# Performance work log

Measured on AMD Instinct MI355X. Metric: run time of the kernel, lower is better.

The kernel has to match this reference:

```python
import jax, jax.numpy as jnp
import numpy as np

B = 16384          # batch
F = 64             # number of feature columns (tables)
L = 10             # pooled lookups per feature (bag size)
E = 16             # embedding dim
V = 1_000_000      # hashed vocab size (shared table)
D = F * E          # concat width = 1024
EPS = 1e-5


def setup_inputs() -> dict:
    key = jax.random.key(0)
    ks = jax.random.split(key, 9)
    idx = jax.random.randint(ks[0], (B, F, L), 0, V, dtype=jnp.int64)
    # NormalTensorInitializer(var=0.01) -> std 0.1
    emb = jax.random.normal(ks[1], (V, E), dtype=jnp.float32) * 0.1
    W1 = jax.random.normal(ks[2], (D, 1024), dtype=jnp.float32) / np.sqrt(D).astype(np.float32)
    b1 = jnp.zeros((1024,), jnp.float32)
    W2 = jax.random.normal(ks[3], (1024, 512), dtype=jnp.float32) / np.sqrt(1024).astype(np.float32)
    b2 = jnp.zeros((512,), jnp.float32)
    W3 = jax.random.normal(ks[4], (512, 1), dtype=jnp.float32) / np.sqrt(512).astype(np.float32)
    b3 = jnp.zeros((1,), jnp.float32)
    return {"idx": idx, "emb": emb, "W1": W1, "b1": b1,
            "W2": W2, "b2": b2, "W3": W3, "b3": b3}


def reference(idx, emb, W1, b1, W2, b2, W3, b3):
    # EmbeddingSumConcat: gather [B,F,L,E], sum-pool over bag dim, concat features
    pooled = jnp.take(emb, idx, axis=0).sum(axis=2)          # [B, F, E]
    x = pooled.reshape(B, D)                                  # [B, F*E]
    # ms.nn.Normalization: per-feature batch standardization
    mu = x.mean(axis=0, keepdims=True)
    var = x.var(axis=0, keepdims=True)
    x = (x - mu) * jax.lax.rsqrt(var + EPS)
    # Dense tower 1024 -> 1024 -> 512 -> 1, sigmoid
    h = jax.nn.relu(x @ W1 + b1)
    h = jax.nn.relu(h @ W2 + b2)
    out = jax.nn.sigmoid(h @ W3 + b3)                         # [B, 1]
    return out
```

## Files before the change

### kernel.cpp

```cpp
#include <hip/hip_runtime.h>
#include <hip/hip_bf16.h>
#include <math.h>

typedef __attribute__((ext_vector_type(8))) short  short8;
typedef __attribute__((ext_vector_type(4))) float  f32x4;
typedef __attribute__((ext_vector_type(4))) unsigned short u16x4;
typedef __attribute__((ext_vector_type(8))) unsigned short u16x8;

#define BATCH 16384
#define NF    64
#define BAGL  10
#define ED    16
#define DW    1024

static __device__ __forceinline__ unsigned short f2bf(float f) {
    unsigned int u = __builtin_bit_cast(unsigned int, f);
    unsigned int r = (u + 0x7fffu + ((u >> 16) & 1u)) >> 16;
    return (unsigned short)r;
}
static __device__ __forceinline__ float bf2f(unsigned short h) {
    unsigned int u = ((unsigned int)h) << 16;
    return __builtin_bit_cast(float, u);
}

__global__ __launch_bounds__(256) void pool_kernel(const int* __restrict__ idx,
                                                   const float* __restrict__ emb,
                                                   unsigned short* __restrict__ xb) {
    const int gid = blockIdx.x * 256 + threadIdx.x;
    const int bag = gid >> 2;
    const int q   = gid & 3;
    const int* ip = idx + (long long)bag * BAGL;

    int v[BAGL];
#pragma unroll
    for (int l = 0; l < BAGL; ++l) v[l] = ip[l];

    f32x4 e[BAGL];
#pragma unroll
    for (int l = 0; l < BAGL; ++l)
        e[l] = *(const f32x4*)(emb + (((long long)v[l]) << 4) + (q << 2));

    f32x4 s01 = e[0] + e[1], s23 = e[2] + e[3], s45 = e[4] + e[5],
          s67 = e[6] + e[7], s89 = e[8] + e[9];
    f32x4 t0 = s01 + s23, t1 = s45 + s67;
    f32x4 acc = (t0 + t1) + s89;

    u16x4 o;
#pragma unroll
    for (int j = 0; j < 4; ++j) o[j] = f2bf(acc[j]);
    *(u16x4*)(xb + (((long long)bag) << 4) + (q << 2)) = o;
}

__global__ __launch_bounds__(256) void stats_kernel(const unsigned short* __restrict__ xb,
                                                    float* __restrict__ ssum,
                                                    float* __restrict__ ssq) {
    const int t = threadIdx.x;
    const long long r0 = (long long)blockIdx.x * 128;
    float s[4] = {0, 0, 0, 0}, q[4] = {0, 0, 0, 0};
    for (int r = 0; r < 128; ++r) {
        const u16x4 v = *(const u16x4*)(xb + (r0 + r) * DW + t * 4);
#pragma unroll
        for (int j = 0; j < 4; ++j) { float f = bf2f(v[j]); s[j] += f; q[j] += f * f; }
    }
#pragma unroll
    for (int j = 0; j < 4; ++j) {
        atomicAdd(&ssum[t * 4 + j], s[j]);
        atomicAdd(&ssq [t * 4 + j], q[j]);
    }
}

__global__ void finalize_stats(const float* __restrict__ ssum, const float* __restrict__ ssq,
                               float* __restrict__ mean, float* __restrict__ rsig) {
    const int c = blockIdx.x * 256 + threadIdx.x;
    const float m = ssum[c] * (1.0f / (float)BATCH);
    const float v = ssq[c] * (1.0f / (float)BATCH) - m * m;
    mean[c] = m;
    rsig[c] = rsqrtf(v + 1e-5f);
}

__global__ __launch_bounds__(256) void normalize_kernel(unsigned short* __restrict__ xb,
                                                        const float* __restrict__ mean,
                                                        const float* __restrict__ rsig) {
    const long long gid = (long long)blockIdx.x * 256 + threadIdx.x;
    const long long off = gid * 8;
    const int c0 = (int)(off & (DW - 1));
    u16x8 v = *(u16x8*)(xb + off);
#pragma unroll
    for (int j = 0; j < 8; ++j) {
        float f = (bf2f(v[j]) - mean[c0 + j]) * rsig[c0 + j];
        v[j] = f2bf(f);
    }
    *(u16x8*)(xb + off) = v;
}

__global__ __launch_bounds__(256) void transpose_f32_bf16(const float* __restrict__ src,
                                                          unsigned short* __restrict__ dst,
                                                          int R, int C) {
    __shared__ float tile[32][33];
    const int tx = threadIdx.x & 31, ty = threadIdx.x >> 5;
    const int bx = blockIdx.x, by = blockIdx.y;
#pragma unroll
    for (int i = 0; i < 4; ++i) {
        const int r = by * 32 + ty + i * 8, c = bx * 32 + tx;
        tile[ty + i * 8][tx] = src[(long long)r * C + c];
    }
    __syncthreads();
#pragma unroll
    for (int i = 0; i < 4; ++i) {
        const int oc = bx * 32 + ty + i * 8;
        dst[(long long)oc * R + by * 32 + tx] = f2bf(tile[tx][ty + i * 8]);
    }
}

template <int RELU>
__global__ __launch_bounds__(256) void gemm_bt(const unsigned short* __restrict__ A,
                                               const unsigned short* __restrict__ Bt,
                                               const float* __restrict__ bias,
                                               unsigned short* __restrict__ C,
                                               int M, int N, int K) {
    __shared__ __align__(16) unsigned short As[128 * 32];
    __shared__ __align__(16) unsigned short Bs[128 * 32];
    const int tid = threadIdx.x;
    const int w = tid >> 6, l = tid & 63;
    const int wr = w >> 1, wc = w & 1;
    const int bm = blockIdx.x, bn = blockIdx.y;
    const int l15 = l & 15, l4 = l >> 4;

    f32x4 acc[4][4] = {};

    const long long a_base = (long long)bm * 128 * K;
    const long long b_base = (long long)bn * 128 * K;

    for (int k0 = 0; k0 < K; k0 += 32) {
#pragma unroll
        for (int i = 0; i < 2; ++i) {
            const int fl = i * 256 + tid;
            const int row = fl >> 2, kq = (fl & 3) << 3;
            __builtin_amdgcn_global_load_lds(
                (const __attribute__((address_space(1))) void*)(A + a_base + (long long)row * K + k0 + kq),
                (__attribute__((address_space(3))) void*)(&As[fl * 8]), 16, 0, 0);
            __builtin_amdgcn_global_load_lds(
                (const __attribute__((address_space(1))) void*)(Bt + b_base + (long long)row * K + k0 + kq),
                (__attribute__((address_space(3))) void*)(&Bs[fl * 8]), 16, 0, 0);
        }
        __syncthreads();

        short8 a[4], b[4];
#pragma unroll
        for (int m = 0; m < 4; ++m)
            a[m] = *(const short8*)(As + (wr * 64 + m * 16 + l15) * 32 + l4 * 8);
#pragma unroll
        for (int n = 0; n < 4; ++n)
            b[n] = *(const short8*)(Bs + (wc * 64 + n * 16 + l15) * 32 + l4 * 8);
#pragma unroll
        for (int m = 0; m < 4; ++m)
#pragma unroll
            for (int n = 0; n < 4; ++n)
                acc[m][n] = __builtin_amdgcn_mfma_f32_16x16x32_bf16(a[m], b[n], acc[m][n], 0, 0, 0);
        __syncthreads();
    }

#pragma unroll
    for (int m = 0; m < 4; ++m) {
        const int grow_base = bm * 128 + wr * 64 + m * 16 + l4 * 4;
#pragma unroll
        for (int n = 0; n < 4; ++n) {
            const int gcol = bn * 128 + wc * 64 + n * 16 + l15;
            const float bv = bias[gcol];
#pragma unroll
            for (int j = 0; j < 4; ++j) {
                float v = acc[m][n][j] + bv;
                if (RELU) v = fmaxf(v, 0.0f);
                C[(long long)(grow_base + j) * N + gcol] = f2bf(v);
            }
        }
    }
}

__global__ __launch_bounds__(256) void final_kernel(const unsigned short* __restrict__ h2,
                                                    const float* __restrict__ W3,
                                                    const float* __restrict__ b3,
                                                    float* __restrict__ out) {
    __shared__ float w3s[512];
    const int tid = threadIdx.x;
    w3s[tid] = W3[tid];
    w3s[tid + 256] = W3[tid + 256];
    __syncthreads();
    const int wv = tid >> 6, l = tid & 63;
    const long long row = (long long)blockIdx.x * 4 + wv;
    const u16x8 h = *(const u16x8*)(h2 + row * 512 + l * 8);
    float acc = 0.f;
#pragma unroll
    for (int j = 0; j < 8; ++j) acc += bf2f(h[j]) * w3s[l * 8 + j];
#pragma unroll
    for (int off = 32; off > 0; off >>= 1) acc += __shfl_xor(acc, off, 64);
    if (l == 0) out[row] = 1.0f / (1.0f + expf(-(acc + b3[0])));
}

extern "C" void kernel_launch(void* const* d_in, const int* in_sizes, int n_in,
                              void* d_out, int out_size, void* d_ws, size_t ws_size,
                              hipStream_t stream) {
    const int*   idx = (const int*)d_in[0];
    const float* emb = (const float*)d_in[1];
    const float* W1  = (const float*)d_in[2];
    const float* b1  = (const float*)d_in[3];
    const float* W2  = (const float*)d_in[4];
    const float* b2  = (const float*)d_in[5];
    const float* W3  = (const float*)d_in[6];
    const float* b3  = (const float*)d_in[7];
    float* out = (float*)d_out;

    char* ws = (char*)d_ws;
    unsigned short* xb  = (unsigned short*)ws; ws += (size_t)BATCH * DW * 2;
    unsigned short* h1  = (unsigned short*)ws; ws += (size_t)BATCH * DW * 2;
    unsigned short* h2  = (unsigned short*)ws; ws += (size_t)BATCH * 512 * 2;
    unsigned short* w1t = (unsigned short*)ws; ws += (size_t)1024 * 1024 * 2;
    unsigned short* w2t = (unsigned short*)ws; ws += (size_t)512 * 1024 * 2;
    float* ssum = (float*)ws; ws += 4096;
    float* ssq  = (float*)ws; ws += 4096;
    float* mean = (float*)ws; ws += 4096;
    float* rsig = (float*)ws; ws += 4096;

    hipMemsetAsync(ssum, 0, 8192, stream);

    pool_kernel<<<(BATCH * NF * 4) / 256, 256, 0, stream>>>(idx, emb, xb);
    stats_kernel<<<BATCH / 128, 256, 0, stream>>>(xb, ssum, ssq);
    finalize_stats<<<4, 256, 0, stream>>>(ssum, ssq, mean, rsig);
    normalize_kernel<<<(BATCH * DW / 8) / 256, 256, 0, stream>>>(xb, mean, rsig);

    transpose_f32_bf16<<<dim3(32, 32), 256, 0, stream>>>(W1, w1t, 1024, 1024);
    transpose_f32_bf16<<<dim3(16, 32), 256, 0, stream>>>(W2, w2t, 1024, 512);

    gemm_bt<1><<<dim3(BATCH / 128, 1024 / 128), 256, 0, stream>>>(xb, w1t, b1, h1, BATCH, 1024, 1024);
    gemm_bt<1><<<dim3(BATCH / 128, 512 / 128), 256, 0, stream>>>(h1, w2t, b2, h2, BATCH, 512, 1024);

    final_kernel<<<BATCH / 4, 256, 0, stream>>>(h2, W3, b3, out);
}
```

Baseline: 328.1 us.

## Fold normalization into W1, fuse final layer into GEMM2, pool from bf16 table

Several changes land together. The batch normalization is folded algebraically into the W1 weights and a corrected bias, which removes the separate normalize pass. The last dense layer is fused into GEMM2's epilogue using atomic row reductions, so h2 is never written out. The GEMMs move to a K=64 tile with XCD-aware block remapping. The embedding table is converted to bf16 on every call before pooling, which adds a full pass over the table (about 64MB read, 32MB written) in exchange for halving gather bytes.

```diff
diff --git a/kernel.cpp b/kernel.cpp
--- a/kernel.cpp
+++ b/kernel.cpp
@@ -12,6 +12,7 @@
 #define BAGL  10
 #define ED    16
 #define DW    1024
+#define VOCAB 1000000
 
 static __device__ __forceinline__ unsigned short f2bf(float f) {
     unsigned int u = __builtin_bit_cast(unsigned int, f);
@@ -23,32 +24,44 @@
     return __builtin_bit_cast(float, u);
 }
 
-__global__ __launch_bounds__(256) void pool_kernel(const int* __restrict__ idx,
-                                                   const float* __restrict__ emb,
-                                                   unsigned short* __restrict__ xb) {
+__global__ __launch_bounds__(256) void emb_to_bf16(const float* __restrict__ e,
+                                                   unsigned short* __restrict__ o) {
+    const long long i = ((long long)blockIdx.x * 256 + threadIdx.x) * 8;
+    if (i >= (long long)VOCAB * ED) return;
+    const f32x4 a = *(const f32x4*)(e + i);
+    const f32x4 b = *(const f32x4*)(e + i + 4);
+    u16x8 r;
+#pragma unroll
+    for (int j = 0; j < 4; ++j) { r[j] = f2bf(a[j]); r[4 + j] = f2bf(b[j]); }
+    *(u16x8*)(o + i) = r;
+}
+
+__global__ __launch_bounds__(256) void pool_bf16(const int* __restrict__ idx,
+                                                 const unsigned short* __restrict__ embb,
+                                                 unsigned short* __restrict__ xb) {
     const int gid = blockIdx.x * 256 + threadIdx.x;
-    const int bag = gid >> 2;
-    const int q   = gid & 3;
+    const int bag = gid >> 1;
+    const int h   = gid & 1;
     const int* ip = idx + (long long)bag * BAGL;
 
     int v[BAGL];
 #pragma unroll
     for (int l = 0; l < BAGL; ++l) v[l] = ip[l];
-
-    f32x4 e[BAGL];
+    u16x8 e[BAGL];
 #pragma unroll
     for (int l = 0; l < BAGL; ++l)
-        e[l] = *(const f32x4*)(emb + (((long long)v[l]) << 4) + (q << 2));
-
-    f32x4 s01 = e[0] + e[1], s23 = e[2] + e[3], s45 = e[4] + e[5],
-          s67 = e[6] + e[7], s89 = e[8] + e[9];
-    f32x4 t0 = s01 + s23, t1 = s45 + s67;
-    f32x4 acc = (t0 + t1) + s89;
-
-    u16x4 o;
-#pragma unroll
-    for (int j = 0; j < 4; ++j) o[j] = f2bf(acc[j]);
-    *(u16x4*)(xb + (((long long)bag) << 4) + (q << 2)) = o;
+        e[l] = *(const u16x8*)(embb + (((long long)v[l]) << 4) + h * 8);
+
+    float s[8] = {0, 0, 0, 0, 0, 0, 0, 0};
+#pragma unroll
+    for (int l = 0; l < BAGL; ++l)
+#pragma unroll
+        for (int j = 0; j < 8; ++j) s[j] += bf2f(e[l][j]);
+
+    u16x8 o;
+#pragma unroll
+    for (int j = 0; j < 8; ++j) o[j] = f2bf(s[j]);
+    *(u16x8*)(xb + (((long long)bag) << 4) + h * 8) = o;
 }
 
 __global__ __launch_bounds__(256) void stats_kernel(const unsigned short* __restrict__ xb,
@@ -70,39 +83,29 @@
 }
 
 __global__ void finalize_stats(const float* __restrict__ ssum, const float* __restrict__ ssq,
-                               float* __restrict__ mean, float* __restrict__ rsig) {
+                               float* __restrict__ mean, float* __restrict__ rsig,
+                               float* __restrict__ murs) {
     const int c = blockIdx.x * 256 + threadIdx.x;
     const float m = ssum[c] * (1.0f / (float)BATCH);
     const float v = ssq[c] * (1.0f / (float)BATCH) - m * m;
-    mean[c] = m;
-    rsig[c] = rsqrtf(v + 1e-5f);
-}
-
-__global__ __launch_bounds__(256) void normalize_kernel(unsigned short* __restrict__ xb,
-                                                        const float* __restrict__ mean,
-                                                        const float* __restrict__ rsig) {
-    const long long gid = (long long)blockIdx.x * 256 + threadIdx.x;
-    const long long off = gid * 8;
-    const int c0 = (int)(off & (DW - 1));
-    u16x8 v = *(u16x8*)(xb + off);
-#pragma unroll
-    for (int j = 0; j < 8; ++j) {
-        float f = (bf2f(v[j]) - mean[c0 + j]) * rsig[c0 + j];
-        v[j] = f2bf(f);
-    }
-    *(u16x8*)(xb + off) = v;
-}
-
+    const float r = rsqrtf(v + 1e-5f);
+    mean[c] = m; rsig[c] = r; murs[c] = m * r;
+}
+
+template <int SCALE>
 __global__ __launch_bounds__(256) void transpose_f32_bf16(const float* __restrict__ src,
                                                           unsigned short* __restrict__ dst,
-                                                          int R, int C) {
+                                                          int R, int C,
+                                                          const float* __restrict__ rs) {
     __shared__ float tile[32][33];
     const int tx = threadIdx.x & 31, ty = threadIdx.x >> 5;
     const int bx = blockIdx.x, by = blockIdx.y;
 #pragma unroll
     for (int i = 0; i < 4; ++i) {
         const int r = by * 32 + ty + i * 8, c = bx * 32 + tx;
-        tile[ty + i * 8][tx] = src[(long long)r * C + c];
+        float v = src[(long long)r * C + c];
+        if (SCALE) v *= rs[r];
+        tile[ty + i * 8][tx] = v;
     }
     __syncthreads();
 #pragma unroll
@@ -112,89 +115,171 @@
     }
 }
 
-template <int RELU>
-__global__ __launch_bounds__(256) void gemm_bt(const unsigned short* __restrict__ A,
-                                               const unsigned short* __restrict__ Bt,
-                                               const float* __restrict__ bias,
-                                               unsigned short* __restrict__ C,
-                                               int M, int N, int K) {
-    __shared__ __align__(16) unsigned short As[128 * 32];
-    __shared__ __align__(16) unsigned short Bs[128 * 32];
+__global__ __launch_bounds__(256) void b1fold_kernel(const float* __restrict__ W1,
+                                                     const float* __restrict__ murs,
+                                                     float* __restrict__ b1n) {
+    const int n = blockIdx.x * 256 + threadIdx.x;
+    const int k0 = blockIdx.y * 128;
+    float acc = 0.f;
+#pragma unroll 4
+    for (int k = 0; k < 128; ++k)
+        acc += murs[k0 + k] * W1[(long long)(k0 + k) * 1024 + n];
+    atomicAdd(&b1n[n], -acc);
+}
+
+__global__ __launch_bounds__(256) void gemm_relu(const unsigned short* __restrict__ A,
+                                                 const unsigned short* __restrict__ Bt,
+                                                 const float* __restrict__ bias,
+                                                 const float* __restrict__ bias2,
+                                                 unsigned short* __restrict__ C,
+                                                 int M, int N, int K, int NBN) {
+    __shared__ __align__(16) unsigned short As[128 * 64];
+    __shared__ __align__(16) unsigned short Bs[128 * 64];
     const int tid = threadIdx.x;
     const int w = tid >> 6, l = tid & 63;
     const int wr = w >> 1, wc = w & 1;
-    const int bm = blockIdx.x, bn = blockIdx.y;
+    const int blk = blockIdx.x, xcd = blk & 7, j = blk >> 3;
+    const int bm = xcd * 16 + j / NBN, bn = j % NBN;
     const int l15 = l & 15, l4 = l >> 4;
 
     f32x4 acc[4][4] = {};
-
     const long long a_base = (long long)bm * 128 * K;
     const long long b_base = (long long)bn * 128 * K;
 
-    for (int k0 = 0; k0 < K; k0 += 32) {
-#pragma unroll
-        for (int i = 0; i < 2; ++i) {
-            const int fl = i * 256 + tid;
-            const int row = fl >> 2, kq = (fl & 3) << 3;
+    for (int k0 = 0; k0 < K; k0 += 64) {
+#pragma unroll
+        for (int i = 0; i < 4; ++i) {
+            const int cid = i * 256 + tid;
+            const int row = cid >> 3, kq = (cid & 7) << 3;
             __builtin_amdgcn_global_load_lds(
                 (const __attribute__((address_space(1))) void*)(A + a_base + (long long)row * K + k0 + kq),
-                (__attribute__((address_space(3))) void*)(&As[fl * 8]), 16, 0, 0);
+                (__attribute__((address_space(3))) void*)(&As[cid * 8]), 16, 0, 0);
             __builtin_amdgcn_global_load_lds(
                 (const __attribute__((address_space(1))) void*)(Bt + b_base + (long long)row * K + k0 + kq),
-                (__attribute__((address_space(3))) void*)(&Bs[fl * 8]), 16, 0, 0);
+                (__attribute__((address_space(3))) void*)(&Bs[cid * 8]), 16, 0, 0);
         }
         __syncthreads();
 
-        short8 a[4], b[4];
-#pragma unroll
-        for (int m = 0; m < 4; ++m)
-            a[m] = *(const short8*)(As + (wr * 64 + m * 16 + l15) * 32 + l4 * 8);
-#pragma unroll
-        for (int n = 0; n < 4; ++n)
-            b[n] = *(const short8*)(Bs + (wc * 64 + n * 16 + l15) * 32 + l4 * 8);
-#pragma unroll
-        for (int m = 0; m < 4; ++m)
+        short8 a[2][4], b[2][4];
+#pragma unroll
+        for (int kk = 0; kk < 2; ++kk) {
+#pragma unroll
+            for (int m = 0; m < 4; ++m)
+                a[kk][m] = *(const short8*)(As + (wr * 64 + m * 16 + l15) * 64 + kk * 32 + l4 * 8);
 #pragma unroll
             for (int n = 0; n < 4; ++n)
-                acc[m][n] = __builtin_amdgcn_mfma_f32_16x16x32_bf16(a[m], b[n], acc[m][n], 0, 0, 0);
+                b[kk][n] = *(const short8*)(Bs + (wc * 64 + n * 16 + l15) * 64 + kk * 32 + l4 * 8);
+        }
+#pragma unroll
+        for (int kk = 0; kk < 2; ++kk)
+#pragma unroll
+            for (int m = 0; m < 4; ++m)
+#pragma unroll
+                for (int n = 0; n < 4; ++n)
+                    acc[m][n] = __builtin_amdgcn_mfma_f32_16x16x32_bf16(a[kk][m], b[kk][n], acc[m][n], 0, 0, 0);
         __syncthreads();
     }
 
 #pragma unroll
     for (int m = 0; m < 4; ++m) {
         const int grow_base = bm * 128 + wr * 64 + m * 16 + l4 * 4;
+#pragma unroll
+        for (int n = 0; n < 4; ++n) {
+            const int gcol = bn * 128 + wc * 64 + n * 16 + l15;
+            const float bv = bias[gcol] + (bias2 ? bias2[gcol] : 0.f);
+#pragma unroll
+            for (int j2 = 0; j2 < 4; ++j2) {
+                float v = fmaxf(acc[m][n][j2] + bv, 0.f);
+                C[(long long)(grow_base + j2) * N + gcol] = f2bf(v);
+            }
+        }
+    }
+}
+
+__global__ __launch_bounds__(256) void gemm2_fused(const unsigned short* __restrict__ A,
+                                                   const unsigned short* __restrict__ Bt,
+                                                   const float* __restrict__ bias,
+                                                   const float* __restrict__ W3,
+                                                   float* __restrict__ logits,
+                                                   int M, int N, int K, int NBN) {
+    __shared__ __align__(16) unsigned short As[128 * 64];
+    __shared__ __align__(16) unsigned short Bs[128 * 64];
+    const int tid = threadIdx.x;
+    const int w = tid >> 6, l = tid & 63;
+    const int wr = w >> 1, wc = w & 1;
+    const int blk = blockIdx.x, xcd = blk & 7, j = blk >> 3;
+    const int bm = xcd * 16 + j / NBN, bn = j % NBN;
+    const int l15 = l & 15, l4 = l >> 4;
+
+    f32x4 acc[4][4] = {};
+    const long long a_base = (long long)bm * 128 * K;
+    const long long b_base = (long long)bn * 128 * K;
+
+    for (int k0 = 0; k0 < K; k0 += 64) {
+#pragma unroll
+        for (int i = 0; i < 4; ++i) {
+            const int cid = i * 256 + tid;
+            const int row = cid >> 3, kq = (cid & 7) << 3;
+            __builtin_amdgcn_global_load_lds(
+                (const __attribute__((address_space(1))) void*)(A + a_base + (long long)row * K + k0 + kq),
+                (__attribute__((address_space(3))) void*)(&As[cid * 8]), 16, 0, 0);
+            __builtin_amdgcn_global_load_lds(
+                (const __attribute__((address_space(1))) void*)(Bt + b_base + (long long)row * K + k0 + kq),
+                (__attribute__((address_space(3))) void*)(&Bs[cid * 8]), 16, 0, 0);
+        }
+        __syncthreads();
+
+        short8 a[2][4], b[2][4];
+#pragma unroll
+        for (int kk = 0; kk < 2; ++kk) {
+#pragma unroll
+            for (int m = 0; m < 4; ++m)
+                a[kk][m] = *(const short8*)(As + (wr * 64 + m * 16 + l15) * 64 + kk * 32 + l4 * 8);
+#pragma unroll
+            for (int n = 0; n < 4; ++n)
+                b[kk][n] = *(const short8*)(Bs + (wc * 64 + n * 16 + l15) * 64 + kk * 32 + l4 * 8);
+        }
+#pragma unroll
+        for (int kk = 0; kk < 2; ++kk)
+#pragma unroll
+            for (int m = 0; m < 4; ++m)
+#pragma unroll
+                for (int n = 0; n < 4; ++n)
+                    acc[m][n] = __builtin_amdgcn_mfma_f32_16x16x32_bf16(a[kk][m], b[kk][n], acc[m][n], 0, 0, 0);
+        __syncthreads();
+    }
+
+#pragma unroll
+    for (int m = 0; m < 4; ++m) {
+        float part[4] = {0.f, 0.f, 0.f, 0.f};
 #pragma unroll
         for (int n = 0; n < 4; ++n) {
             const int gcol = bn * 128 + wc * 64 + n * 16 + l15;
             const float bv = bias[gcol];
-#pragma unroll
-            for (int j = 0; j < 4; ++j) {
-                float v = acc[m][n][j] + bv;
-                if (RELU) v = fmaxf(v, 0.0f);
-                C[(long long)(grow_base + j) * N + gcol] = f2bf(v);
+            const float w3 = W3[gcol];
+#pragma unroll
+            for (int j2 = 0; j2 < 4; ++j2) {
+                float v = fmaxf(acc[m][n][j2] + bv, 0.f);
+                part[j2] += v * w3;
             }
         }
-    }
-}
-
-__global__ __launch_bounds__(256) void final_kernel(const unsigned short* __restrict__ h2,
-                                                    const float* __restrict__ W3,
-                                                    const float* __restrict__ b3,
-                                                    float* __restrict__ out) {
-    __shared__ float w3s[512];
-    const int tid = threadIdx.x;
-    w3s[tid] = W3[tid];
-    w3s[tid + 256] = W3[tid + 256];
-    __syncthreads();
-    const int wv = tid >> 6, l = tid & 63;
-    const long long row = (long long)blockIdx.x * 4 + wv;
-    const u16x8 h = *(const u16x8*)(h2 + row * 512 + l * 8);
-    float acc = 0.f;
-#pragma unroll
-    for (int j = 0; j < 8; ++j) acc += bf2f(h[j]) * w3s[l * 8 + j];
-#pragma unroll
-    for (int off = 32; off > 0; off >>= 1) acc += __shfl_xor(acc, off, 64);
-    if (l == 0) out[row] = 1.0f / (1.0f + expf(-(acc + b3[0])));
+#pragma unroll
+        for (int off = 1; off < 16; off <<= 1)
+#pragma unroll
+            for (int j2 = 0; j2 < 4; ++j2) part[j2] += __shfl_xor(part[j2], off, 64);
+        if (l15 == 0) {
+            const int grow = bm * 128 + wr * 64 + m * 16 + l4 * 4;
+#pragma unroll
+            for (int j2 = 0; j2 < 4; ++j2) atomicAdd(&logits[grow + j2], part[j2]);
+        }
+    }
+}
+
+__global__ __launch_bounds__(256) void sigmoid_kernel(const float* __restrict__ logits,
+                                                      const float* __restrict__ b3,
+                                                      float* __restrict__ out) {
+    const int i = blockIdx.x * 256 + threadIdx.x;
+    out[i] = 1.0f / (1.0f + expf(-(logits[i] + b3[0])));
 }
 
 extern "C" void kernel_launch(void* const* d_in, const int* in_sizes, int n_in,
@@ -210,29 +295,39 @@
     const float* b3  = (const float*)d_in[7];
     float* out = (float*)d_out;
 
+    const size_t EMBB_H1_BYTES = (size_t)BATCH * DW * 2;
+
     char* ws = (char*)d_ws;
-    unsigned short* xb  = (unsigned short*)ws; ws += (size_t)BATCH * DW * 2;
-    unsigned short* h1  = (unsigned short*)ws; ws += (size_t)BATCH * DW * 2;
-    unsigned short* h2  = (unsigned short*)ws; ws += (size_t)BATCH * 512 * 2;
-    unsigned short* w1t = (unsigned short*)ws; ws += (size_t)1024 * 1024 * 2;
-    unsigned short* w2t = (unsigned short*)ws; ws += (size_t)512 * 1024 * 2;
-    float* ssum = (float*)ws; ws += 4096;
-    float* ssq  = (float*)ws; ws += 4096;
-    float* mean = (float*)ws; ws += 4096;
-    float* rsig = (float*)ws; ws += 4096;
-
-    hipMemsetAsync(ssum, 0, 8192, stream);
-
-    pool_kernel<<<(BATCH * NF * 4) / 256, 256, 0, stream>>>(idx, emb, xb);
+    unsigned short* xb   = (unsigned short*)ws; ws += (size_t)BATCH * DW * 2;
+    unsigned short* embb = (unsigned short*)ws; ws += EMBB_H1_BYTES;
+    unsigned short* h1   = embb;
+    unsigned short* w1t  = (unsigned short*)ws; ws += (size_t)1024 * 1024 * 2;
+    unsigned short* w2t  = (unsigned short*)ws; ws += (size_t)512 * 1024 * 2;
+    float* ssum   = (float*)ws; ws += 4096;
+    float* ssq    = (float*)ws; ws += 4096;
+    float* b1n    = (float*)ws; ws += 4096;
+    float* logits = (float*)ws; ws += (size_t)BATCH * 4;
+    float* mean   = (float*)ws; ws += 4096;
+    float* rsig   = (float*)ws; ws += 4096;
+    float* murs   = (float*)ws; ws += 4096;
+
+    hipMemsetAsync(ssum, 0, 4096 * 3 + (size_t)BATCH * 4, stream);
+
+    const long long embElems = (long long)VOCAB * ED;
+    const int embBlocks = (int)((embElems / 8 + 255) / 256);
+    emb_to_bf16<<<embBlocks, 256, 0, stream>>>(emb, embb);
+    pool_bf16<<<(BATCH * NF * 2) / 256, 256, 0, stream>>>(idx, embb, xb);
     stats_kernel<<<BATCH / 128, 256, 0, stream>>>(xb, ssum, ssq);
-    finalize_stats<<<4, 256, 0, stream>>>(ssum, ssq, mean, rsig);
-    normalize_kernel<<<(BATCH * DW / 8) / 256, 256, 0, stream>>>(xb, mean, rsig);
-
-    transpose_f32_bf16<<<dim3(32, 32), 256, 0, stream>>>(W1, w1t, 1024, 1024);
-    transpose_f32_bf16<<<dim3(16, 32), 256, 0, stream>>>(W2, w2t, 1024, 512);
-
-    gemm_bt<1><<<dim3(BATCH / 128, 1024 / 128), 256, 0, stream>>>(xb, w1t, b1, h1, BATCH, 1024, 1024);
-    gemm_bt<1><<<dim3(BATCH / 128, 512 / 128), 256, 0, stream>>>(h1, w2t, b2, h2, BATCH, 512, 1024);
-
-    final_kernel<<<BATCH / 4, 256, 0, stream>>>(h2, W3, b3, out);
-}
+    finalize_stats<<<4, 256, 0, stream>>>(ssum, ssq, mean, rsig, murs);
+
+    transpose_f32_bf16<1><<<dim3(32, 32), 256, 0, stream>>>(W1, w1t, 1024, 1024, rsig);
+    b1fold_kernel<<<dim3(4, 8), 256, 0, stream>>>(W1, murs, b1n);
+    transpose_f32_bf16<0><<<dim3(16, 32), 256, 0, stream>>>(W2, w2t, 1024, 512, nullptr);
+
+    gemm_relu<<<(BATCH / 128) * (1024 / 128), 256, 0, stream>>>(
+        xb, w1t, b1, b1n, h1, BATCH, 1024, 1024, 1024 / 128);
+    gemm2_fused<<<(BATCH / 128) * (512 / 128), 256, 0, stream>>>(
+        h1, w2t, b2, W3, logits, BATCH, 512, 1024, 512 / 128);
+
+    sigmoid_kernel<<<BATCH / 256, 256, 0, stream>>>(logits, b3, out);
+}
```

Measured after the change: 325.8 us. No clear change (-0.7%).
